# Kernel optimization log

Hardware: AMD Instinct MI355X
Metric: run time of the kernel (lower is better)

The kernel has to match this reference:

```python
import jax, jax.numpy as jnp
import numpy as np

E = 8        # num_experts
TOP_K = 2
DIM = 1024
DFF = DIM // 4
T = 32768    # batch*seq tokens


def setup_inputs() -> dict:
    key = jax.random.key(0)
    ks = jax.random.split(key, 5)
    x = jax.random.normal(ks[0], (T, DIM), dtype=jnp.float32)
    router_w = jax.random.normal(ks[1], (E, DIM), dtype=jnp.float32) * 0.02
    w1 = jax.random.normal(ks[2], (E, DIM, DFF), dtype=jnp.float32) * 0.02
    w2 = jax.random.normal(ks[3], (E, DFF, DIM), dtype=jnp.float32) * 0.02
    w3 = jax.random.normal(ks[4], (E, DIM, DFF), dtype=jnp.float32) * 0.02
    return {"x": x, "router_w": router_w, "w1": w1, "w2": w2, "w3": w3}


def reference(x, router_w, w1, w2, w3):
    # ---- Router ----
    logits = x @ router_w.T                          # [T, E]
    scores = jax.nn.softmax(logits.astype(jnp.float32), axis=1)
    # expert_bias is zero at init and noise_scale=0 -> topk on raw scores
    _, sel = jax.lax.top_k(scores, TOP_K)            # [T, K] expert indices
    top_scores = jnp.take_along_axis(scores, sel, axis=-1)
    top_scores = top_scores / jnp.sum(top_scores, axis=-1, keepdims=True)

    flat_experts = sel.reshape(-1)                   # [T*K]
    sorted_idx = jnp.argsort(flat_experts)           # stable sort, expert-centric order
    scatter_idx = sorted_idx // TOP_K                # original token id per row
    num_tokens_per_expert = jnp.bincount(flat_experts, length=E).astype(jnp.int32)

    x_gathered = x[scatter_idx]                      # [T*K, DIM]
    scores_sorted = top_scores.reshape(-1)[sorted_idx]  # [T*K]

    # ---- GroupedExpert: grouped GEMM SwiGLU in bf16 ----
    xb = x_gathered.astype(jnp.bfloat16)
    x1 = jax.lax.ragged_dot(xb, w1.astype(jnp.bfloat16), num_tokens_per_expert)
    x3 = jax.lax.ragged_dot(xb, w3.astype(jnp.bfloat16), num_tokens_per_expert)
    h = jax.nn.silu(x1) * x3                         # [T*K, DFF] bf16
    expert_out = jax.lax.ragged_dot(h, w2.astype(jnp.bfloat16), num_tokens_per_expert)
    expert_out = expert_out.astype(x.dtype)          # [T*K, DIM]

    # ---- Combine: weighted scatter-add back to token positions ----
    out = jnp.zeros_like(x).at[scatter_idx].add(expert_out * scores_sorted[:, None])
    return out
```

## Files before the change

### kernel.cpp

```cpp
#include <hip/hip_runtime.h>
#include <cstdint>
#include <cstddef>
#include <math.h>

#define T_TOK 32768
#define DIM   1024
#define DFF   256
#define NE    8
#define NB    16
#define ROWS  (T_TOK * 2)
#define MAXROWS 66560
#define MAXTILES (MAXROWS / 64)

typedef unsigned short u16;
typedef __attribute__((ext_vector_type(8))) short v8s;
typedef __attribute__((ext_vector_type(4))) float v4f;

__device__ __forceinline__ u16 f2bf(float f) {
  union { float f; unsigned u; } v; v.f = f;
  return (u16)((v.u + 0x7FFFu + ((v.u >> 16) & 1u)) >> 16);
}
__device__ __forceinline__ float bf2f(u16 b) {
  union { unsigned u; float f; } v; v.u = ((unsigned)b) << 16; return v.f;
}

#define WS_W13  ((size_t)0)
#define WS_W2T  ((size_t)8388608)
#define WS_H    ((size_t)12582912)
#define WS_Y    ((size_t)46661632)
#define WS_RTOK ((size_t)182976512)
#define WS_POS  ((size_t)183242752)
#define WS_CNT  ((size_t)183504896)
#define WS_CUR  ((size_t)183504960)
#define WS_OFF  ((size_t)183505024)
#define WS_SEL  ((size_t)183505152)
#define WS_WTS  ((size_t)183767296)

__global__ __launch_bounds__(256) void k_pack13(const float* __restrict__ w1,
                                                const float* __restrict__ w3,
                                                u16* __restrict__ W13p) {
  __shared__ float s1[32][33];
  __shared__ float s3[32][33];
  int e = blockIdx.z, k0 = blockIdx.x * 32, j0w = blockIdx.y;
  int tx = threadIdx.x, ty = threadIdx.y;
  size_t wbase = (size_t)e * DIM * DFF;
#pragma unroll
  for (int r = 0; r < 4; ++r) {
    int kl = ty + 8 * r;
    size_t src = wbase + (size_t)(k0 + kl) * DFF + j0w * 32 + tx;
    s1[kl][tx] = w1[src];
    s3[kl][tx] = w3[src];
  }
  __syncthreads();
  size_t obase = (size_t)e * 512 * 1024;
#pragma unroll
  for (int r = 0; r < 4; ++r) {
    int jl = ty + 8 * r;
    int n1 = 64 * j0w + jl;
    W13p[obase + (size_t)n1 * 1024 + k0 + tx]        = f2bf(s1[tx][jl]);
    W13p[obase + (size_t)(n1 + 32) * 1024 + k0 + tx] = f2bf(s3[tx][jl]);
  }
}

__global__ __launch_bounds__(256) void k_pack2(const float* __restrict__ w2,
                                               u16* __restrict__ W2t) {
  __shared__ float s[32][33];
  int e = blockIdx.z, k0 = blockIdx.x * 32, n0 = blockIdx.y * 32;
  int tx = threadIdx.x, ty = threadIdx.y;
#pragma unroll
  for (int r = 0; r < 4; ++r) {
    int kl = ty + 8 * r;
    s[kl][tx] = w2[(size_t)e * DFF * DIM + (size_t)(k0 + kl) * DIM + n0 + tx];
  }
  __syncthreads();
#pragma unroll
  for (int r = 0; r < 4; ++r) {
    int nl = ty + 8 * r;
    W2t[(size_t)e * DIM * DFF + (size_t)(n0 + nl) * DFF + k0 + tx] = f2bf(s[tx][nl]);
  }
}

__global__ __launch_bounds__(256) void k_router(const float* __restrict__ x,
                                                const float* __restrict__ rw,
                                                int* __restrict__ sel,
                                                float* __restrict__ wts,
                                                int* __restrict__ cnt) {
  __shared__ __align__(16) float s_rw[NE][1028];
  __shared__ __align__(16) float s_x[32][132];
  __shared__ float s_lg[256];
  __shared__ int s_cnt[NB];
  int tid = threadIdx.x;
  if (tid < NB) s_cnt[tid] = 0;
  {
    const float4* rw4 = (const float4*)rw;
#pragma unroll
    for (int r = 0; r < 8; ++r)
      *(float4*)(&s_rw[r][tid * 4]) = rw4[r * 256 + tid];
  }
  int tl = tid >> 3, e = tid & 7;
  float acc = 0.0f;
  const float4* x4 = (const float4*)x;
  for (int c = 0; c < 8; ++c) {
    __syncthreads();
#pragma unroll
    for (int j = 0; j < 4; ++j) {
      int slot = j * 256 + tid;
      int t = slot >> 5, kk = (slot & 31) * 4;
      *(float4*)(&s_x[t][kk]) = x4[((size_t)blockIdx.x * 32 + t) * 256 + c * 32 + (slot & 31)];
    }
    __syncthreads();
    const float* xp = &s_x[tl][0];
    const float* wp = &s_rw[e][c * 128];
#pragma unroll 16
    for (int k = 0; k < 128; ++k) acc = fmaf(xp[k], wp[k], acc);
  }
  s_lg[tid] = acc;
  __syncthreads();
  if ((tid & 7) == 0) {
    int t = blockIdx.x * 32 + tl;
    const float* lg = s_lg + tid;
    int b0 = 0; float v0 = lg[0];
#pragma unroll
    for (int ee = 1; ee < NE; ++ee) if (lg[ee] > v0) { v0 = lg[ee]; b0 = ee; }
    int b1 = -1; float v1 = -1e30f;
#pragma unroll
    for (int ee = 0; ee < NE; ++ee) if (ee != b0 && lg[ee] > v1) { v1 = lg[ee]; b1 = ee; }
    float w0 = 1.0f / (1.0f + expf(v1 - v0));
    sel[2 * t] = b0; sel[2 * t + 1] = b1;
    wts[2 * t] = w0; wts[2 * t + 1] = 1.0f - w0;
    atomicAdd(&s_cnt[2 * b0], 1);
    atomicAdd(&s_cnt[2 * b1 + 1], 1);
  }
  __syncthreads();
  if (tid < NB && s_cnt[tid]) atomicAdd(&cnt[tid], s_cnt[tid]);
}

__global__ void k_scan(const int* __restrict__ cnt, int* __restrict__ offs) {
  if (threadIdx.x == 0 && blockIdx.x == 0) {
    int o = 0;
#pragma unroll
    for (int b = 0; b < NB; ++b) { offs[b] = o; o += (cnt[b] + 63) & ~63; }
    offs[NB] = o;
  }
}

__global__ __launch_bounds__(256) void k_scatter(const int* __restrict__ sel,
                                                 const int* __restrict__ offs,
                                                 int* __restrict__ cursor,
                                                 int* __restrict__ rtok,
                                                 int* __restrict__ pos) {
  __shared__ int s_cnt[NB], s_base[NB];
  int tid = threadIdx.x;
  if (tid < NB) s_cnt[tid] = 0;
  __syncthreads();
  int g = blockIdx.x * 256 + tid;
  int b = sel[g] * 2 + (g & 1);
  int lpos = atomicAdd(&s_cnt[b], 1);
  __syncthreads();
  if (tid < NB) s_base[tid] = s_cnt[tid] ? atomicAdd(&cursor[tid], s_cnt[tid]) : 0;
  __syncthreads();
  int row = offs[b] + s_base[b] + lpos;
  rtok[row] = g >> 1;
  pos[g] = row;
}

__global__ __launch_bounds__(512, 4) void k_gemm1(const float* __restrict__ x,
                                                  const u16* __restrict__ W13p,
                                                  const int* __restrict__ rtok,
                                                  const int* __restrict__ offs,
                                                  u16* __restrict__ h) {
  __shared__ __align__(16) u16 A_s[64][40];
  __shared__ __align__(16) u16 B_s[512][40];
  int row0 = blockIdx.x * 64;
  if (row0 >= offs[NB]) return;
  int b2 = 0;
  while (row0 >= offs[b2 + 1]) ++b2;
  int e = b2 >> 1;
  int tid = threadIdx.x;
  int ar = tid >> 3, ac = (tid & 7) * 4;
  int tk = rtok[row0 + ar];
  if (tk < 0) tk = 0;
  const float* xrow = x + (size_t)tk * DIM;
  const u16* Bb = W13p + (size_t)e * 512 * 1024;
  int wv = tid >> 6, lane = tid & 63;
  int lr = lane & 15, q = lane >> 4;
  v4f acc[4][4] = {};
  for (int k0 = 0; k0 < DIM; k0 += 32) {
    float4 xv = *(const float4*)(xrow + k0 + ac);
    ushort4 a4;
    a4.x = f2bf(xv.x); a4.y = f2bf(xv.y); a4.z = f2bf(xv.z); a4.w = f2bf(xv.w);
    *(ushort4*)(&A_s[ar][ac]) = a4;
#pragma unroll
    for (int qq = 0; qq < 4; ++qq) {
      int id = qq * 512 + tid;
      int n = id >> 2, c8 = (id & 3) * 8;
      *(uint4*)(&B_s[n][c8]) = *(const uint4*)(Bb + (size_t)n * 1024 + k0 + c8);
    }
    __syncthreads();
    v8s a[4], b[4];
#pragma unroll
    for (int mt = 0; mt < 4; ++mt) a[mt] = *(const v8s*)(&A_s[16 * mt + lr][q * 8]);
#pragma unroll
    for (int nt = 0; nt < 4; ++nt) b[nt] = *(const v8s*)(&B_s[64 * wv + 16 * nt + lr][q * 8]);
#pragma unroll
    for (int mt = 0; mt < 4; ++mt)
#pragma unroll
      for (int nt = 0; nt < 4; ++nt)
        acc[mt][nt] = __builtin_amdgcn_mfma_f32_16x16x32_bf16(a[mt], b[nt], acc[mt][nt], 0, 0, 0);
    __syncthreads();
  }
#pragma unroll
  for (int mt = 0; mt < 4; ++mt)
#pragma unroll
    for (int nt = 0; nt < 2; ++nt)
#pragma unroll
      for (int r = 0; r < 4; ++r) {
        float x1 = bf2f(f2bf(acc[mt][nt][r]));
        float x3 = bf2f(f2bf(acc[mt][nt + 2][r]));
        float hv = x1 * x3 / (1.0f + __expf(-x1));
        int row = row0 + 16 * mt + q * 4 + r;
        int col = 32 * wv + 16 * nt + lr;
        h[(size_t)row * DFF + col] = f2bf(hv);
      }
}

__global__ __launch_bounds__(512, 4) void k_gemm2(const u16* __restrict__ h,
                                                  const u16* __restrict__ W2t,
                                                  const int* __restrict__ offs,
                                                  u16* __restrict__ y) {
  __shared__ __align__(16) u16 A_s[64][40];
  __shared__ __align__(16) u16 B_s[512][40];
  int row0 = blockIdx.x * 64;
  if (row0 >= offs[NB]) return;
  int b2 = 0;
  while (row0 >= offs[b2 + 1]) ++b2;
  int e = b2 >> 1;
  int nb = blockIdx.y;
  int tid = threadIdx.x;
  int ar = tid >> 3, ac = (tid & 7) * 4;
  const u16* hrow = h + (size_t)(row0 + ar) * DFF;
  const u16* Bb = W2t + (size_t)e * DIM * DFF + (size_t)nb * 512 * DFF;
  int wv = tid >> 6, lane = tid & 63;
  int lr = lane & 15, q = lane >> 4;
  v4f acc[4][4] = {};
  for (int k0 = 0; k0 < DFF; k0 += 32) {
    *(ushort4*)(&A_s[ar][ac]) = *(const ushort4*)(hrow + k0 + ac);
#pragma unroll
    for (int qq = 0; qq < 4; ++qq) {
      int id = qq * 512 + tid;
      int n = id >> 2, c8 = (id & 3) * 8;
      *(uint4*)(&B_s[n][c8]) = *(const uint4*)(Bb + (size_t)n * DFF + k0 + c8);
    }
    __syncthreads();
    v8s a[4], b[4];
#pragma unroll
    for (int mt = 0; mt < 4; ++mt) a[mt] = *(const v8s*)(&A_s[16 * mt + lr][q * 8]);
#pragma unroll
    for (int nt = 0; nt < 4; ++nt) b[nt] = *(const v8s*)(&B_s[64 * wv + 16 * nt + lr][q * 8]);
#pragma unroll
    for (int mt = 0; mt < 4; ++mt)
#pragma unroll
      for (int nt = 0; nt < 4; ++nt)
        acc[mt][nt] = __builtin_amdgcn_mfma_f32_16x16x32_bf16(a[mt], b[nt], acc[mt][nt], 0, 0, 0);
    __syncthreads();
  }
  u16* Ts = &B_s[0][0];
#pragma unroll
  for (int mt = 0; mt < 4; ++mt) {
#pragma unroll
    for (int nt = 0; nt < 4; ++nt)
#pragma unroll
      for (int r = 0; r < 4; ++r)
        Ts[(q * 4 + r) * 520 + 64 * wv + 16 * nt + lr] = f2bf(acc[mt][nt][r]);
    __syncthreads();
#pragma unroll
    for (int i = 0; i < 2; ++i) {
      int j = tid + 512 * i;
      int rr = j >> 6, cc = j & 63;
      uint4 v = *(const uint4*)(Ts + rr * 520 + cc * 8);
      *(uint4*)(y + (size_t)(row0 + 16 * mt + rr) * 1024 + nb * 512 + cc * 8) = v;
    }
    __syncthreads();
  }
}

__global__ __launch_bounds__(256) void k_combine(const u16* __restrict__ y,
                                                 const int* __restrict__ pos,
                                                 const float* __restrict__ wts,
                                                 float* __restrict__ out) {
  int tid = threadIdx.x, wv = tid >> 6, lane = tid & 63;
  int t = blockIdx.x * 4 + wv;
  int r0 = pos[2 * t], r1 = pos[2 * t + 1];
  float w0 = wts[2 * t], w1 = wts[2 * t + 1];
  const uint4* y0 = (const uint4*)(y + (size_t)r0 * 1024);
  const uint4* y1 = (const uint4*)(y + (size_t)r1 * 1024);
  float* o = out + (size_t)t * 1024;
#pragma unroll
  for (int i = 0; i < 2; ++i) {
    int j = lane + 64 * i;
    uint4 a = y0[j], b = y1[j];
    const u16* pa = (const u16*)&a;
    const u16* pb = (const u16*)&b;
    float f[8];
#pragma unroll
    for (int k = 0; k < 8; ++k) f[k] = bf2f(pa[k]) * w0 + bf2f(pb[k]) * w1;
    *(float4*)(o + j * 8)     = *(float4*)&f[0];
    *(float4*)(o + j * 8 + 4) = *(float4*)&f[4];
  }
}

extern "C" void kernel_launch(void* const* d_in, const int* in_sizes, int n_in,
                              void* d_out, int out_size, void* d_ws, size_t ws_size,
                              hipStream_t stream) {
  (void)in_sizes; (void)n_in; (void)ws_size; (void)out_size;
  const float* x  = (const float*)d_in[0];
  const float* rw = (const float*)d_in[1];
  const float* w1 = (const float*)d_in[2];
  const float* w2 = (const float*)d_in[3];
  const float* w3 = (const float*)d_in[4];
  float* out = (float*)d_out;
  char* ws = (char*)d_ws;
  u16*   W13p = (u16*)(ws + WS_W13);
  u16*   W2t  = (u16*)(ws + WS_W2T);
  u16*   hbuf = (u16*)(ws + WS_H);
  u16*   ybuf = (u16*)(ws + WS_Y);
  int*   rtok = (int*)(ws + WS_RTOK);
  int*   pos  = (int*)(ws + WS_POS);
  int*   cnt  = (int*)(ws + WS_CNT);
  int*   cur  = (int*)(ws + WS_CUR);
  int*   offs = (int*)(ws + WS_OFF);
  int*   sel  = (int*)(ws + WS_SEL);
  float* wts  = (float*)(ws + WS_WTS);

  hipMemsetAsync(ws + WS_RTOK, 0xFF, (size_t)MAXROWS * 4, stream);
  hipMemsetAsync(ws + WS_CNT, 0, 128, stream);

  k_pack13<<<dim3(32, 8, 8), dim3(32, 8), 0, stream>>>(w1, w3, W13p);
  k_pack2 <<<dim3(8, 32, 8), dim3(32, 8), 0, stream>>>(w2, W2t);
  k_router<<<dim3(T_TOK / 32), dim3(256), 0, stream>>>(x, rw, sel, wts, cnt);
  k_scan  <<<dim3(1), dim3(64), 0, stream>>>(cnt, offs);
  k_scatter<<<dim3(ROWS / 256), dim3(256), 0, stream>>>(sel, offs, cur, rtok, pos);
  k_gemm1 <<<dim3(MAXTILES), dim3(512), 0, stream>>>(x, W13p, rtok, offs, hbuf);
  k_gemm2 <<<dim3(MAXTILES, 2), dim3(512), 0, stream>>>(hbuf, W2t, offs, ybuf);
  k_combine<<<dim3(T_TOK / 4), dim3(256), 0, stream>>>(ybuf, pos, wts, out);
}
```

Before: 524.3 us.

## Pre-convert x to bf16 in router and use direct global-to-LDS loads in GEMMs

The router kernel now also writes a bf16 copy of x into workspace reused from the y buffer, so gemm1 no longer reads fp32 x and converts it per tile. Both GEMMs replace register-staged tile loads with global_load_lds 16-byte direct-to-LDS transfers into unpadded tiles. The tiles use an XOR swizzle so the MFMA fragment reads avoid bank conflicts. Block indices are remapped so tiles are interleaved across groups of eight. This cuts gemm1's A-side traffic and load instructions, but adds a bf16 write of x in the router and depends on the swizzle and LDS layout being exactly right.

```diff
diff --git a/kernel.cpp b/kernel.cpp
--- a/kernel.cpp
+++ b/kernel.cpp
@@ -22,6 +22,12 @@
 }
 __device__ __forceinline__ float bf2f(u16 b) {
   union { unsigned u; float f; } v; v.u = ((unsigned)b) << 16; return v.f;
+}
+
+__device__ __forceinline__ void gload16(const u16* g, u16* l) {
+  __builtin_amdgcn_global_load_lds(
+      (const __attribute__((address_space(1))) void*)g,
+      (__attribute__((address_space(3))) void*)l, 16, 0, 0);
 }
 
 #define WS_W13  ((size_t)0)
@@ -35,6 +41,7 @@
 #define WS_OFF  ((size_t)183505024)
 #define WS_SEL  ((size_t)183505152)
 #define WS_WTS  ((size_t)183767296)
+#define WS_XB   WS_Y
 
 __global__ __launch_bounds__(256) void k_pack13(const float* __restrict__ w1,
                                                 const float* __restrict__ w3,
@@ -84,7 +91,8 @@
                                                 const float* __restrict__ rw,
                                                 int* __restrict__ sel,
                                                 float* __restrict__ wts,
-                                                int* __restrict__ cnt) {
+                                                int* __restrict__ cnt,
+                                                u16* __restrict__ xb) {
   __shared__ __align__(16) float s_rw[NE][1028];
   __shared__ __align__(16) float s_x[32][132];
   __shared__ float s_lg[256];
@@ -113,6 +121,16 @@
     const float* wp = &s_rw[e][c * 128];
 #pragma unroll 16
     for (int k = 0; k < 128; ++k) acc = fmaf(xp[k], wp[k], acc);
+    {
+      int t2 = tid >> 3, k2 = (tid & 7) * 16;
+      const float* sp = &s_x[t2][k2];
+      u16 tb[16];
+#pragma unroll
+      for (int k = 0; k < 16; ++k) tb[k] = f2bf(sp[k]);
+      u16* xo = xb + ((size_t)(blockIdx.x * 32 + t2)) * 1024 + c * 128 + k2;
+      *(uint4*)(xo)     = *(const uint4*)(&tb[0]);
+      *(uint4*)(xo + 8) = *(const uint4*)(&tb[8]);
+    }
   }
   s_lg[tid] = acc;
   __syncthreads();
@@ -164,44 +182,44 @@
   pos[g] = row;
 }
 
-__global__ __launch_bounds__(512, 4) void k_gemm1(const float* __restrict__ x,
+__global__ __launch_bounds__(512, 4) void k_gemm1(const u16* __restrict__ xb,
                                                   const u16* __restrict__ W13p,
                                                   const int* __restrict__ rtok,
                                                   const int* __restrict__ offs,
                                                   u16* __restrict__ h) {
-  __shared__ __align__(16) u16 A_s[64][40];
-  __shared__ __align__(16) u16 B_s[512][40];
-  int row0 = blockIdx.x * 64;
+  __shared__ __align__(16) u16 A_s[64][32];
+  __shared__ __align__(16) u16 B_s[512][32];
+  int bx = (int)((blockIdx.x & 7) * (MAXTILES / 8) + (blockIdx.x >> 3));
+  int row0 = bx * 64;
   if (row0 >= offs[NB]) return;
   int b2 = 0;
   while (row0 >= offs[b2 + 1]) ++b2;
   int e = b2 >> 1;
   int tid = threadIdx.x;
-  int ar = tid >> 3, ac = (tid & 7) * 4;
-  int tk = rtok[row0 + ar];
-  if (tk < 0) tk = 0;
-  const float* xrow = x + (size_t)tk * DIM;
-  const u16* Bb = W13p + (size_t)e * 512 * 1024;
   int wv = tid >> 6, lane = tid & 63;
   int lr = lane & 15, q = lane >> 4;
+  int qa = q ^ ((lr >> 1) & 3);
+  int srow = lane >> 2;
+  int schk = (lane & 3) ^ ((lane >> 3) & 3);
+  const u16* srcB = W13p + (size_t)e * 512 * 1024
+                  + (size_t)(64 * wv + srow) * 1024 + schk * 8;
+  int arow = (wv >= 4) ? (16 * (wv - 4) + srow) : srow;
+  int tk = rtok[row0 + arow]; if (tk < 0) tk = 0;
+  const u16* srcA = xb + (size_t)tk * 1024 + schk * 8;
+  u16* ldsB = &B_s[64 * wv][0];
+  u16* ldsA = &A_s[(wv & 3) * 16][0];
   v4f acc[4][4] = {};
   for (int k0 = 0; k0 < DIM; k0 += 32) {
-    float4 xv = *(const float4*)(xrow + k0 + ac);
-    ushort4 a4;
-    a4.x = f2bf(xv.x); a4.y = f2bf(xv.y); a4.z = f2bf(xv.z); a4.w = f2bf(xv.w);
-    *(ushort4*)(&A_s[ar][ac]) = a4;
-#pragma unroll
-    for (int qq = 0; qq < 4; ++qq) {
-      int id = qq * 512 + tid;
-      int n = id >> 2, c8 = (id & 3) * 8;
-      *(uint4*)(&B_s[n][c8]) = *(const uint4*)(Bb + (size_t)n * 1024 + k0 + c8);
-    }
+#pragma unroll
+    for (int i = 0; i < 4; ++i)
+      gload16(srcB + (size_t)i * 16 * 1024 + k0, ldsB + i * 512);
+    if (wv >= 4) gload16(srcA + k0, ldsA);
     __syncthreads();
     v8s a[4], b[4];
 #pragma unroll
-    for (int mt = 0; mt < 4; ++mt) a[mt] = *(const v8s*)(&A_s[16 * mt + lr][q * 8]);
-#pragma unroll
-    for (int nt = 0; nt < 4; ++nt) b[nt] = *(const v8s*)(&B_s[64 * wv + 16 * nt + lr][q * 8]);
+    for (int mt = 0; mt < 4; ++mt) a[mt] = *(const v8s*)(&A_s[16 * mt + lr][qa * 8]);
+#pragma unroll
+    for (int nt = 0; nt < 4; ++nt) b[nt] = *(const v8s*)(&B_s[64 * wv + 16 * nt + lr][qa * 8]);
 #pragma unroll
     for (int mt = 0; mt < 4; ++mt)
 #pragma unroll
@@ -228,35 +246,39 @@
                                                   const u16* __restrict__ W2t,
                                                   const int* __restrict__ offs,
                                                   u16* __restrict__ y) {
-  __shared__ __align__(16) u16 A_s[64][40];
-  __shared__ __align__(16) u16 B_s[512][40];
-  int row0 = blockIdx.x * 64;
+  __shared__ __align__(16) u16 A_s[64][32];
+  __shared__ __align__(16) u16 B_s[512][32];
+  int bx = (int)((blockIdx.x & 7) * (MAXTILES / 8) + (blockIdx.x >> 3));
+  int row0 = bx * 64;
   if (row0 >= offs[NB]) return;
   int b2 = 0;
   while (row0 >= offs[b2 + 1]) ++b2;
   int e = b2 >> 1;
   int nb = blockIdx.y;
   int tid = threadIdx.x;
-  int ar = tid >> 3, ac = (tid & 7) * 4;
-  const u16* hrow = h + (size_t)(row0 + ar) * DFF;
-  const u16* Bb = W2t + (size_t)e * DIM * DFF + (size_t)nb * 512 * DFF;
   int wv = tid >> 6, lane = tid & 63;
   int lr = lane & 15, q = lane >> 4;
+  int qa = q ^ ((lr >> 1) & 3);
+  int srow = lane >> 2;
+  int schk = (lane & 3) ^ ((lane >> 3) & 3);
+  const u16* srcB = W2t + (size_t)e * DIM * DFF + (size_t)nb * 512 * DFF
+                  + (size_t)(64 * wv + srow) * DFF + schk * 8;
+  int arow = (wv >= 4) ? (16 * (wv - 4) + srow) : srow;
+  const u16* srcA = h + (size_t)(row0 + arow) * DFF + schk * 8;
+  u16* ldsB = &B_s[64 * wv][0];
+  u16* ldsA = &A_s[(wv & 3) * 16][0];
   v4f acc[4][4] = {};
   for (int k0 = 0; k0 < DFF; k0 += 32) {
-    *(ushort4*)(&A_s[ar][ac]) = *(const ushort4*)(hrow + k0 + ac);
-#pragma unroll
-    for (int qq = 0; qq < 4; ++qq) {
-      int id = qq * 512 + tid;
-      int n = id >> 2, c8 = (id & 3) * 8;
-      *(uint4*)(&B_s[n][c8]) = *(const uint4*)(Bb + (size_t)n * DFF + k0 + c8);
-    }
+#pragma unroll
+    for (int i = 0; i < 4; ++i)
+      gload16(srcB + (size_t)i * 16 * DFF + k0, ldsB + i * 512);
+    if (wv >= 4) gload16(srcA + k0, ldsA);
     __syncthreads();
     v8s a[4], b[4];
 #pragma unroll
-    for (int mt = 0; mt < 4; ++mt) a[mt] = *(const v8s*)(&A_s[16 * mt + lr][q * 8]);
-#pragma unroll
-    for (int nt = 0; nt < 4; ++nt) b[nt] = *(const v8s*)(&B_s[64 * wv + 16 * nt + lr][q * 8]);
+    for (int mt = 0; mt < 4; ++mt) a[mt] = *(const v8s*)(&A_s[16 * mt + lr][qa * 8]);
+#pragma unroll
+    for (int nt = 0; nt < 4; ++nt) b[nt] = *(const v8s*)(&B_s[64 * wv + 16 * nt + lr][qa * 8]);
 #pragma unroll
     for (int mt = 0; mt < 4; ++mt)
 #pragma unroll
@@ -324,6 +346,7 @@
   u16*   W2t  = (u16*)(ws + WS_W2T);
   u16*   hbuf = (u16*)(ws + WS_H);
   u16*   ybuf = (u16*)(ws + WS_Y);
+  u16*   xbuf = (u16*)(ws + WS_XB);
   int*   rtok = (int*)(ws + WS_RTOK);
   int*   pos  = (int*)(ws + WS_POS);
   int*   cnt  = (int*)(ws + WS_CNT);
@@ -337,10 +360,10 @@
 
   k_pack13<<<dim3(32, 8, 8), dim3(32, 8), 0, stream>>>(w1, w3, W13p);
   k_pack2 <<<dim3(8, 32, 8), dim3(32, 8), 0, stream>>>(w2, W2t);
-  k_router<<<dim3(T_TOK / 32), dim3(256), 0, stream>>>(x, rw, sel, wts, cnt);
+  k_router<<<dim3(T_TOK / 32), dim3(256), 0, stream>>>(x, rw, sel, wts, cnt, xbuf);
   k_scan  <<<dim3(1), dim3(64), 0, stream>>>(cnt, offs);
   k_scatter<<<dim3(ROWS / 256), dim3(256), 0, stream>>>(sel, offs, cur, rtok, pos);
-  k_gemm1 <<<dim3(MAXTILES), dim3(512), 0, stream>>>(x, W13p, rtok, offs, hbuf);
+  k_gemm1 <<<dim3(MAXTILES), dim3(512), 0, stream>>>(xbuf, W13p, rtok, offs, hbuf);
   k_gemm2 <<<dim3(MAXTILES, 2), dim3(512), 0, stream>>>(hbuf, W2t, offs, ybuf);
   k_combine<<<dim3(T_TOK / 4), dim3(256), 0, stream>>>(ybuf, pos, wts, out);
 }
```

Result: faster. 494.1 us (-5.8%).
